# Kernel optimization log

Measured on AMD Instinct MI355X. Metric: run time of the kernel, lower is better.

## Reference

```python
import jax, jax.numpy as jnp
import numpy as np

B, S, D, H = 4, 4096, 512, 512


def setup_inputs() -> dict:
    key = jax.random.key(0)
    ks = jax.random.split(key, 11)
    def rn(k, shape):
        return jax.random.normal(k, shape, dtype=jnp.float32)
    return {
        "query": rn(ks[0], (B, 1, D)),
        "keys": rn(ks[1], (B, S, D)),
        "values": rn(ks[2], (B, S, D)),
        "Wq": rn(ks[3], (D, H)) / np.sqrt(D),
        "bq": rn(ks[4], (H,)) * 0.02,
        "Wk": rn(ks[5], (D, H)) / np.sqrt(D),
        "bk": rn(ks[6], (H,)) * 0.02,
        "Wv": rn(ks[7], (D, H)) / np.sqrt(D),
        "bv": rn(ks[8], (H,)) * 0.02,
        "Wo": rn(ks[9], (H, D)) / np.sqrt(H),
        "bo": rn(ks[10], (D,)) * 0.02,
    }


def reference(query, keys, values, Wq, bq, Wk, bk, Wv, bv, Wo, bo):
    # projections
    q = query @ Wq + bq      # (B, 1, H)
    k = keys @ Wk + bk       # (B, S, H)
    v = values @ Wv + bv     # (B, S, H)
    scale = jnp.sqrt(jnp.asarray(q.shape[-1], dtype=jnp.float32))
    # single-query scores: (B, 1, S)
    scores = jnp.einsum('bqh,bsh->bqs', q, k)
    seq = k.shape[1]
    # torch masked_fill broadcasts (B,1,S) against tril (1,S,S) -> (B,S,S)
    causal = jnp.tril(jnp.ones((seq, seq), dtype=bool))[None]  # (1, S, S)
    masked = jnp.where(causal, scores, -jnp.inf)                # (B, S, S)
    attn_weights = jax.nn.softmax(masked / scale, axis=-1)      # (B, S, S)
    context = jnp.einsum('brs,bsh->brh', attn_weights, v)       # (B, S, H)
    out = context @ Wo + bo                                     # (B, S, D)
    return out, attn_weights
```

## Files before the change

kernel.cpp:

```cpp
#include <hip/hip_runtime.h>
#include <hip/hip_bf16.h>

#define BB 4
#define SS 4096
#define DD 512
#define HH 512

typedef __attribute__((ext_vector_type(8))) short bf16x8;
typedef __attribute__((ext_vector_type(4))) float f32x4;

__global__ __launch_bounds__(256) void k_pre1(const float* __restrict__ query,
                                              const float* __restrict__ Wq,
                                              const float* __restrict__ bq,
                                              const float* __restrict__ Wv,
                                              const float* __restrict__ Wo,
                                              float* __restrict__ qv,
                                              float* __restrict__ Wvop) {
    __shared__ float smem[8320];
    int wb = blockIdx.x, tid = threadIdx.x;
    if (wb < 32) {
        float* qs = smem;
        float (*red)[64] = reinterpret_cast<float(*)[64]>(smem + 512);
        int hg = wb & 7, b = wb >> 3;
        int hl = tid & 63, qq = tid >> 6;
        int h = hg * 64 + hl;
        for (int d = tid; d < DD; d += 256) qs[d] = query[b * DD + d];
        __syncthreads();
        float a = 0.f;
        int d0 = qq * 128;
        for (int d = d0; d < d0 + 128; ++d)
            a += qs[d] * Wq[(size_t)d * HH + h];
        red[qq][hl] = a;
        __syncthreads();
        if (tid < 64)
            qv[b * HH + hg * 64 + tid] = red[0][tid] + red[1][tid] + red[2][tid] + red[3][tid]
                                       + bq[hg * 64 + tid];
    } else {
        int t = wb - 32;
        int hs = t >> 6, rem = t & 63;
        int n0 = (rem & 7) * 64, k0 = (rem >> 3) * 64;
        float (*lo)[65] = reinterpret_cast<float(*)[65]>(smem);
        float (*lv)[65] = reinterpret_cast<float(*)[65]>(smem + 4160);
        int tn = (tid & 15) * 4, tk = (tid >> 4) * 4;
        float acc[4][4] = {};
        int hbase = hs * 128;
        for (int h0 = hbase; h0 < hbase + 128; h0 += 64) {
            for (int i = tid; i < 64 * 64; i += 256) {
                int rr = i >> 6, cc = i & 63;
                lo[rr][cc] = Wo[(size_t)(h0 + rr) * DD + n0 + cc];
                lv[rr][cc] = Wv[(size_t)(k0 + rr) * HH + h0 + cc];
            }
            __syncthreads();
            for (int h = 0; h < 64; ++h)
#pragma unroll
                for (int a = 0; a < 4; ++a) {
                    float vv = lv[tk + a][h];
#pragma unroll
                    for (int c = 0; c < 4; ++c) acc[a][c] += vv * lo[h][tn + c];
                }
            __syncthreads();
        }
        float* dst = Wvop + (size_t)hs * (DD * HH);
        for (int a = 0; a < 4; ++a)
            for (int c = 0; c < 4; ++c)
                dst[(size_t)(k0 + tk + a) * DD + n0 + tn + c] = acc[a][c];
    }
}

__global__ __launch_bounds__(256) void k_pre2(const float* __restrict__ Wk,
                                              const float* __restrict__ qv,
                                              const float* __restrict__ bk,
                                              const float* __restrict__ Wvop,
                                              const float* __restrict__ bv,
                                              const float* __restrict__ Wo,
                                              const float* __restrict__ bo,
                                              float* __restrict__ wout,
                                              float* __restrict__ cq,
                                              __hip_bfloat16* __restrict__ WvoT,
                                              float* __restrict__ bfinal) {
    __shared__ float smem[4160];
    int wb = blockIdx.x, tid = threadIdx.x;
    if (wb < 512) {
        float* qs = smem;
        float* red = smem + 512;
        int b = wb >> 7, dg = wb & 127;
        int wid = tid >> 6, lane = tid & 63;
        for (int h = tid; h < HH; h += 256) qs[h] = qv[b * HH + h];
        __syncthreads();
        int d = dg * 4 + wid;
        const float4* row = reinterpret_cast<const float4*>(Wk + (size_t)d * HH);
        float4 r0 = row[lane * 2], r1 = row[lane * 2 + 1];
        int h = lane * 8;
        float acc = r0.x * qs[h] + r0.y * qs[h + 1] + r0.z * qs[h + 2] + r0.w * qs[h + 3]
                  + r1.x * qs[h + 4] + r1.y * qs[h + 5] + r1.z * qs[h + 6] + r1.w * qs[h + 7];
        for (int off = 32; off > 0; off >>= 1) acc += __shfl_down(acc, off);
        if (lane == 0) wout[b * DD + d] = acc;
        if (dg == 0) {
            red[tid] = qs[tid] * bk[tid] + qs[tid + 256] * bk[tid + 256];
            __syncthreads();
            for (int off = 128; off > 0; off >>= 1) {
                if (tid < off) red[tid] += red[tid + off];
                __syncthreads();
            }
            if (tid == 0) cq[b] = red[0];
        }
    } else if (wb < 576) {
        int t = wb - 512;
        int n0 = (t & 7) * 64, k0 = (t >> 3) * 64;
        float (*ts)[65] = reinterpret_cast<float(*)[65]>(smem);
#pragma unroll
        for (int i = 0; i < 16; ++i) {
            int idx = tid + i * 256;
            int kk = idx >> 6, nn = idx & 63;
            size_t off = (size_t)(k0 + kk) * DD + n0 + nn;
            float s = Wvop[off] + Wvop[(size_t)DD * HH + off]
                    + Wvop[2 * (size_t)DD * HH + off] + Wvop[3 * (size_t)DD * HH + off];
            ts[nn][kk] = s;
        }
        __syncthreads();
#pragma unroll
        for (int i = 0; i < 16; ++i) {
            int idx = tid + i * 256;
            int row = idx >> 6, col = idx & 63;
            WvoT[(size_t)(n0 + row) * DD + k0 + col] = __float2bfloat16(ts[row][col]);
        }
    } else {
        int n0 = (wb - 576) * 64;
        int nn = tid & 63, hs = tid >> 6;
        float acc = 0.f;
        for (int hh = 0; hh < 128; ++hh) {
            int h = hs * 128 + hh;
            acc += bv[h] * Wo[(size_t)h * DD + n0 + nn];
        }
        float (*red)[64] = reinterpret_cast<float(*)[64]>(smem);
        red[hs][nn] = acc;
        __syncthreads();
        if (tid < 64)
            bfinal[n0 + tid] = red[0][tid] + red[1][tid] + red[2][tid] + red[3][tid]
                             + bo[n0 + tid];
    }
}

__global__ __launch_bounds__(256) void k_scores_p(const float* __restrict__ keys,
                                                  const float* __restrict__ wv,
                                                  const float* __restrict__ cq,
                                                  float* __restrict__ p) {
    __shared__ float ws[DD];
    int wb = blockIdx.x, tid = threadIdx.x;
    int b = wb >> 10, sg = wb & 1023;
    int wid = tid >> 6, lane = tid & 63;
    for (int d = tid; d < DD; d += 256) ws[d] = wv[b * DD + d];
    __syncthreads();
    int s = sg * 4 + wid;
    const float4* row = reinterpret_cast<const float4*>(keys + ((size_t)b * SS + s) * DD);
    float4 r0 = row[lane * 2], r1 = row[lane * 2 + 1];
    int h = lane * 8;
    float acc = r0.x * ws[h] + r0.y * ws[h + 1] + r0.z * ws[h + 2] + r0.w * ws[h + 3]
              + r1.x * ws[h + 4] + r1.y * ws[h + 5] + r1.z * ws[h + 6] + r1.w * ws[h + 7];
    for (int off = 32; off > 0; off >>= 1) acc += __shfl_down(acc, off);
    const float inv_scale = 0.04419417382415922f;
    if (lane == 0) p[b * SS + s] = expf((acc + cq[b]) * inv_scale);
}

__global__ __launch_bounds__(64) void k_tile_scan(const float* __restrict__ values,
                                                  const float* __restrict__ p,
                                                  float* __restrict__ T64,
                                                  float* __restrict__ inv_cum) {
    int bx = blockIdx.x, tid = threadIdx.x;
    if (bx < 512) {
        __shared__ float ps[64];
        int b = bx >> 7, t = (bx >> 1) & 63, chunk = bx & 1;
        ps[tid] = p[b * SS + t * 64 + tid];
        __syncthreads();
        int d = chunk * 256 + tid * 4;
        const float* vp = values + ((size_t)b * SS + (size_t)t * 64) * DD + d;
        f32x4 acc = {0.f, 0.f, 0.f, 0.f};
        for (int i = 0; i < 64; ++i) {
            float4 v = *reinterpret_cast<const float4*>(vp + (size_t)i * DD);
            float pi = ps[i];
            acc[0] += pi * v.x; acc[1] += pi * v.y; acc[2] += pi * v.z; acc[3] += pi * v.w;
        }
        *reinterpret_cast<f32x4*>(&T64[((size_t)b * 64 + t) * DD + d]) = acc;
    } else {
        int b = bx - 512;
        const float* pb = p + (size_t)b * SS;
        float loc[64];
        float own = 0.f;
#pragma unroll
        for (int g = 0; g < 16; ++g) {
            float4 v = *reinterpret_cast<const float4*>(pb + tid * 64 + g * 4);
            loc[g * 4 + 0] = v.x; loc[g * 4 + 1] = v.y;
            loc[g * 4 + 2] = v.z; loc[g * 4 + 3] = v.w;
            own += v.x + v.y + v.z + v.w;
        }
        float incl = own;
        for (int off = 1; off < 64; off <<= 1) {
            float v = __shfl_up(incl, off);
            if (tid >= off) incl += v;
        }
        float run = incl - own;
        float* ib = inv_cum + (size_t)b * SS + tid * 64;
#pragma unroll
        for (int g = 0; g < 16; ++g) {
            float4 iv;
            run += loc[g * 4 + 0]; iv.x = 1.f / run;
            run += loc[g * 4 + 1]; iv.y = 1.f / run;
            run += loc[g * 4 + 2]; iv.z = 1.f / run;
            run += loc[g * 4 + 3]; iv.w = 1.f / run;
            *reinterpret_cast<float4*>(ib + g * 4) = iv;
        }
    }
}

__global__ __launch_bounds__(512) void k_fat(const float* __restrict__ values,
                                             const float* __restrict__ p,
                                             const float* __restrict__ icum,
                                             const float* __restrict__ T64,
                                             const __hip_bfloat16* __restrict__ Bt,
                                             const float* __restrict__ bfinal,
                                             float* __restrict__ Out,
                                             float* __restrict__ attn) {
    __shared__ __align__(16) short As[64][512];
    __shared__ float ps[64], ics[64];
    int bx = blockIdx.x, tid = threadIdx.x;
    if (bx < 256) {
        int b = bx >> 6, tb = bx & 63;
        int m0 = bx * 64;
        if (tid < 64) ps[tid] = p[b * SS + tb * 64 + tid];
        else if (tid < 128) ics[tid - 64] = icum[b * SS + tb * 64 + (tid - 64)];
        float acc = 0.f;
        for (int t = 0; t < tb; ++t) acc += T64[((size_t)b * 64 + t) * DD + tid];
        __syncthreads();
        const float* vp = values + ((size_t)b * SS + (size_t)tb * 64) * DD + tid;
        int gcol = tid >> 3, gsub = tid & 7;
        for (int i = 0; i < 64; ++i) {
            acc += ps[i] * vp[(size_t)i * DD];
            __hip_bfloat16 cv = __float2bfloat16(acc * ics[i]);
            short sv;
            __builtin_memcpy(&sv, &cv, 2);
            As[i][(((gcol ^ (i & 7)) << 3) | gsub)] = sv;
        }
        __syncthreads();
        int wv = tid >> 6, lane = tid & 63;
        int n0 = wv * 64;
        int lrow = lane & 15, lk = (lane >> 4) * 8;
        f32x4 oacc[4][4] = {};
        const short* Bp = reinterpret_cast<const short*>(Bt);
        for (int kk = 0; kk < 512; kk += 32) {
            int gbase = (kk + lk) >> 3;
            bf16x8 af[4], bfr[4];
#pragma unroll
            for (int i = 0; i < 4; ++i) {
                int row = i * 16 + lrow;
                af[i] = *reinterpret_cast<const bf16x8*>(&As[row][((gbase ^ (row & 7)) << 3)]);
            }
#pragma unroll
            for (int j = 0; j < 4; ++j)
                bfr[j] = *reinterpret_cast<const bf16x8*>(Bp + (size_t)(n0 + j * 16 + lrow) * 512 + kk + lk);
#pragma unroll
            for (int i = 0; i < 4; ++i)
#pragma unroll
                for (int j = 0; j < 4; ++j)
                    oacc[i][j] = __builtin_amdgcn_mfma_f32_16x16x32_bf16(af[i], bfr[j], oacc[i][j], 0, 0, 0);
        }
        int rbase = (lane >> 4) * 4;
        for (int i = 0; i < 4; ++i)
            for (int j = 0; j < 4; ++j) {
                int col = n0 + j * 16 + lrow;
                float bb = bfinal[col];
#pragma unroll
                for (int r = 0; r < 4; ++r) {
                    int row = m0 + i * 16 + rbase + r;
                    Out[(size_t)row * DD + col] = oacc[i][j][r] + bb;
                }
            }
    } else {
        int ab = bx - 256;
        int b = ab >> 9, rblk = ab & 511;
        int r0 = rblk * 8;
        const float* pb = p + b * SS;
        float4 pv[2];
        pv[0] = *reinterpret_cast<const float4*>(pb + tid * 4);
        pv[1] = *reinterpret_cast<const float4*>(pb + 2048 + tid * 4);
        const float* icb = icum + b * SS + r0;
#pragma unroll
        for (int row = 0; row < 8; ++row) {
            int r = r0 + row;
            float ic = icb[row];
            size_t base = ((size_t)b * SS + r) * SS;
#pragma unroll
            for (int g = 0; g < 2; ++g) {
                int s = g * 2048 + tid * 4;
                float4 o;
                o.x = (s + 0 <= r) ? pv[g].x * ic : 0.f;
                o.y = (s + 1 <= r) ? pv[g].y * ic : 0.f;
                o.z = (s + 2 <= r) ? pv[g].z * ic : 0.f;
                o.w = (s + 3 <= r) ? pv[g].w * ic : 0.f;
                *reinterpret_cast<float4*>(&attn[base + s]) = o;
            }
        }
    }
}

extern "C" void kernel_launch(void* const* d_in, const int* in_sizes, int n_in,
                              void* d_out, int out_size, void* d_ws, size_t ws_size,
                              hipStream_t stream) {
    const float* query  = (const float*)d_in[0];
    const float* keys   = (const float*)d_in[1];
    const float* values = (const float*)d_in[2];
    const float* Wq = (const float*)d_in[3];
    const float* bq = (const float*)d_in[4];
    const float* Wk = (const float*)d_in[5];
    const float* bk = (const float*)d_in[6];
    const float* Wv = (const float*)d_in[7];
    const float* bv = (const float*)d_in[8];
    const float* Wo = (const float*)d_in[9];
    const float* bo = (const float*)d_in[10];

    float* out  = (float*)d_out;
    float* attn = out + (size_t)BB * SS * DD;

    char* ws = (char*)d_ws;
    float* Wvop = (float*)(ws);
    __hip_bfloat16* WvoT = (__hip_bfloat16*)(ws + 4194304);
    float* T64  = (float*)(ws + 4718592);
    float* p    = (float*)(ws + 5242880);
    float* icum = (float*)(ws + 5308416);
    float* qv   = (float*)(ws + 5373952);
    float* wv   = (float*)(ws + 5382144);
    float* cq   = (float*)(ws + 5390336);
    float* bfin = (float*)(ws + 5390592);

    k_pre1     <<<288,   256, 0, stream>>>(query, Wq, bq, Wv, Wo, qv, Wvop);
    k_pre2     <<<584,   256, 0, stream>>>(Wk, qv, bk, Wvop, bv, Wo, bo, wv, cq, WvoT, bfin);
    k_scores_p <<<4096,  256, 0, stream>>>(keys, wv, cq, p);
    k_tile_scan<<<516,    64, 0, stream>>>(values, p, T64, icum);
    k_fat      <<<2304,  512, 0, stream>>>(values, p, icum, T64, WvoT, bfin, out, attn);
}
```

Measured before the change: 115.2 us.

## Merge pre-kernels and scores into fewer launches, widen tile-scan blocks

Computes q, cq and the Wk-projected query vector inside one block per batch in the first kernel, which removes the separate k_pre2 dot-product stage. The score/exp computation is fused into the same launch as the Wvo transpose and the bias reduction, with each block now handling 16 rows. The tile-scan kernel moves to 256-thread blocks covering full rows with float2 loads. This drops one kernel launch and its dependency boundary, but the q/Wk work now runs serially in only four blocks, which may lengthen the critical path.

```diff
diff --git a/kernel.cpp b/kernel.cpp
--- a/kernel.cpp
+++ b/kernel.cpp
@@ -9,34 +9,52 @@
 typedef __attribute__((ext_vector_type(8))) short bf16x8;
 typedef __attribute__((ext_vector_type(4))) float f32x4;
 
-__global__ __launch_bounds__(256) void k_pre1(const float* __restrict__ query,
-                                              const float* __restrict__ Wq,
-                                              const float* __restrict__ bq,
-                                              const float* __restrict__ Wv,
-                                              const float* __restrict__ Wo,
-                                              float* __restrict__ qv,
-                                              float* __restrict__ Wvop) {
+__global__ __launch_bounds__(256) void k_pre(const float* __restrict__ query,
+                                             const float* __restrict__ Wq,
+                                             const float* __restrict__ bq,
+                                             const float* __restrict__ Wk,
+                                             const float* __restrict__ bk,
+                                             const float* __restrict__ Wv,
+                                             const float* __restrict__ Wo,
+                                             float* __restrict__ wout,
+                                             float* __restrict__ cq,
+                                             float* __restrict__ Wvop) {
     __shared__ float smem[8320];
     int wb = blockIdx.x, tid = threadIdx.x;
-    if (wb < 32) {
-        float* qs = smem;
-        float (*red)[64] = reinterpret_cast<float(*)[64]>(smem + 512);
-        int hg = wb & 7, b = wb >> 3;
-        int hl = tid & 63, qq = tid >> 6;
-        int h = hg * 64 + hl;
-        for (int d = tid; d < DD; d += 256) qs[d] = query[b * DD + d];
-        __syncthreads();
-        float a = 0.f;
-        int d0 = qq * 128;
-        for (int d = d0; d < d0 + 128; ++d)
-            a += qs[d] * Wq[(size_t)d * HH + h];
-        red[qq][hl] = a;
-        __syncthreads();
-        if (tid < 64)
-            qv[b * HH + hg * 64 + tid] = red[0][tid] + red[1][tid] + red[2][tid] + red[3][tid]
-                                       + bq[hg * 64 + tid];
+    if (wb < 4) {
+        float* qs  = smem;
+        float* qo  = smem + 512;
+        float* red = smem + 1024;
+        int b = wb;
+        qs[tid] = query[b * DD + tid];
+        qs[tid + 256] = query[b * DD + tid + 256];
+        __syncthreads();
+        float a0 = bq[tid], a1 = bq[tid + 256];
+        for (int d = 0; d < DD; ++d) {
+            float qd = qs[d];
+            a0 += qd * Wq[(size_t)d * HH + tid];
+            a1 += qd * Wq[(size_t)d * HH + tid + 256];
+        }
+        qo[tid] = a0; qo[tid + 256] = a1;
+        red[tid] = a0 * bk[tid] + a1 * bk[tid + 256];
+        __syncthreads();
+        for (int off = 128; off > 0; off >>= 1) {
+            if (tid < off) red[tid] += red[tid + off];
+            __syncthreads();
+        }
+        if (tid == 0) cq[b] = red[0];
+        float w0 = 0.f, w1 = 0.f;
+        const float* wk0 = Wk + (size_t)tid * HH;
+        const float* wk1 = Wk + (size_t)(tid + 256) * HH;
+        for (int h = 0; h < HH; ++h) {
+            float qh = qo[h];
+            w0 += qh * wk0[h];
+            w1 += qh * wk1[h];
+        }
+        wout[b * DD + tid] = w0;
+        wout[b * DD + tid + 256] = w1;
     } else {
-        int t = wb - 32;
+        int t = wb - 4;
         int hs = t >> 6, rem = t & 63;
         int n0 = (rem & 7) * 64, k0 = (rem >> 3) * 64;
         float (*lo)[65] = reinterpret_cast<float(*)[65]>(smem);
@@ -67,45 +85,39 @@
     }
 }
 
-__global__ __launch_bounds__(256) void k_pre2(const float* __restrict__ Wk,
-                                              const float* __restrict__ qv,
-                                              const float* __restrict__ bk,
-                                              const float* __restrict__ Wvop,
-                                              const float* __restrict__ bv,
-                                              const float* __restrict__ Wo,
-                                              const float* __restrict__ bo,
-                                              float* __restrict__ wout,
-                                              float* __restrict__ cq,
-                                              __hip_bfloat16* __restrict__ WvoT,
-                                              float* __restrict__ bfinal) {
+__global__ __launch_bounds__(256) void k_scores_wr(const float* __restrict__ keys,
+                                                   const float* __restrict__ wv,
+                                                   const float* __restrict__ cq,
+                                                   const float* __restrict__ Wvop,
+                                                   const float* __restrict__ bv,
+                                                   const float* __restrict__ Wo,
+                                                   const float* __restrict__ bo,
+                                                   float* __restrict__ p,
+                                                   __hip_bfloat16* __restrict__ WvoT,
+                                                   float* __restrict__ bfinal) {
     __shared__ float smem[4160];
     int wb = blockIdx.x, tid = threadIdx.x;
-    if (wb < 512) {
-        float* qs = smem;
-        float* red = smem + 512;
-        int b = wb >> 7, dg = wb & 127;
+    if (wb < 1024) {
+        float* ws = smem;
+        int b = wb >> 8, sg = wb & 255;
         int wid = tid >> 6, lane = tid & 63;
-        for (int h = tid; h < HH; h += 256) qs[h] = qv[b * HH + h];
-        __syncthreads();
-        int d = dg * 4 + wid;
-        const float4* row = reinterpret_cast<const float4*>(Wk + (size_t)d * HH);
-        float4 r0 = row[lane * 2], r1 = row[lane * 2 + 1];
+        for (int d = tid; d < DD; d += 256) ws[d] = wv[b * DD + d];
+        __syncthreads();
+        const float inv_scale = 0.04419417382415922f;
+        float cqb = cq[b];
         int h = lane * 8;
-        float acc = r0.x * qs[h] + r0.y * qs[h + 1] + r0.z * qs[h + 2] + r0.w * qs[h + 3]
-                  + r1.x * qs[h + 4] + r1.y * qs[h + 5] + r1.z * qs[h + 6] + r1.w * qs[h + 7];
-        for (int off = 32; off > 0; off >>= 1) acc += __shfl_down(acc, off);
-        if (lane == 0) wout[b * DD + d] = acc;
-        if (dg == 0) {
-            red[tid] = qs[tid] * bk[tid] + qs[tid + 256] * bk[tid + 256];
-            __syncthreads();
-            for (int off = 128; off > 0; off >>= 1) {
-                if (tid < off) red[tid] += red[tid + off];
-                __syncthreads();
-            }
-            if (tid == 0) cq[b] = red[0];
-        }
-    } else if (wb < 576) {
-        int t = wb - 512;
+#pragma unroll
+        for (int rr = 0; rr < 4; ++rr) {
+            int s = sg * 16 + wid * 4 + rr;
+            const float4* row = reinterpret_cast<const float4*>(keys + ((size_t)b * SS + s) * DD);
+            float4 r0 = row[lane * 2], r1 = row[lane * 2 + 1];
+            float acc = r0.x * ws[h] + r0.y * ws[h + 1] + r0.z * ws[h + 2] + r0.w * ws[h + 3]
+                      + r1.x * ws[h + 4] + r1.y * ws[h + 5] + r1.z * ws[h + 6] + r1.w * ws[h + 7];
+            for (int off = 32; off > 0; off >>= 1) acc += __shfl_down(acc, off);
+            if (lane == 0) p[b * SS + s] = expf((acc + cqb) * inv_scale);
+        }
+    } else if (wb < 1088) {
+        int t = wb - 1024;
         int n0 = (t & 7) * 64, k0 = (t >> 3) * 64;
         float (*ts)[65] = reinterpret_cast<float(*)[65]>(smem);
 #pragma unroll
@@ -125,7 +137,7 @@
             WvoT[(size_t)(n0 + row) * DD + k0 + col] = __float2bfloat16(ts[row][col]);
         }
     } else {
-        int n0 = (wb - 576) * 64;
+        int n0 = (wb - 1088) * 64;
         int nn = tid & 63, hs = tid >> 6;
         float acc = 0.f;
         for (int hh = 0; hh < 128; ++hh) {
@@ -141,48 +153,27 @@
     }
 }
 
-__global__ __launch_bounds__(256) void k_scores_p(const float* __restrict__ keys,
-                                                  const float* __restrict__ wv,
-                                                  const float* __restrict__ cq,
-                                                  float* __restrict__ p) {
-    __shared__ float ws[DD];
-    int wb = blockIdx.x, tid = threadIdx.x;
-    int b = wb >> 10, sg = wb & 1023;
-    int wid = tid >> 6, lane = tid & 63;
-    for (int d = tid; d < DD; d += 256) ws[d] = wv[b * DD + d];
-    __syncthreads();
-    int s = sg * 4 + wid;
-    const float4* row = reinterpret_cast<const float4*>(keys + ((size_t)b * SS + s) * DD);
-    float4 r0 = row[lane * 2], r1 = row[lane * 2 + 1];
-    int h = lane * 8;
-    float acc = r0.x * ws[h] + r0.y * ws[h + 1] + r0.z * ws[h + 2] + r0.w * ws[h + 3]
-              + r1.x * ws[h + 4] + r1.y * ws[h + 5] + r1.z * ws[h + 6] + r1.w * ws[h + 7];
-    for (int off = 32; off > 0; off >>= 1) acc += __shfl_down(acc, off);
-    const float inv_scale = 0.04419417382415922f;
-    if (lane == 0) p[b * SS + s] = expf((acc + cq[b]) * inv_scale);
-}
-
-__global__ __launch_bounds__(64) void k_tile_scan(const float* __restrict__ values,
-                                                  const float* __restrict__ p,
-                                                  float* __restrict__ T64,
-                                                  float* __restrict__ inv_cum) {
+__global__ __launch_bounds__(256) void k_tile_scan(const float* __restrict__ values,
+                                                   const float* __restrict__ p,
+                                                   float* __restrict__ T64,
+                                                   float* __restrict__ inv_cum) {
     int bx = blockIdx.x, tid = threadIdx.x;
-    if (bx < 512) {
+    if (bx < 256) {
         __shared__ float ps[64];
-        int b = bx >> 7, t = (bx >> 1) & 63, chunk = bx & 1;
-        ps[tid] = p[b * SS + t * 64 + tid];
-        __syncthreads();
-        int d = chunk * 256 + tid * 4;
-        const float* vp = values + ((size_t)b * SS + (size_t)t * 64) * DD + d;
-        f32x4 acc = {0.f, 0.f, 0.f, 0.f};
+        int b = bx >> 6, t = bx & 63;
+        if (tid < 64) ps[tid] = p[b * SS + t * 64 + tid];
+        __syncthreads();
+        const float* vp = values + ((size_t)b * SS + (size_t)t * 64) * DD + tid * 2;
+        float ax = 0.f, ay = 0.f;
         for (int i = 0; i < 64; ++i) {
-            float4 v = *reinterpret_cast<const float4*>(vp + (size_t)i * DD);
+            float2 v = *reinterpret_cast<const float2*>(vp + (size_t)i * DD);
             float pi = ps[i];
-            acc[0] += pi * v.x; acc[1] += pi * v.y; acc[2] += pi * v.z; acc[3] += pi * v.w;
-        }
-        *reinterpret_cast<f32x4*>(&T64[((size_t)b * 64 + t) * DD + d]) = acc;
-    } else {
-        int b = bx - 512;
+            ax += pi * v.x; ay += pi * v.y;
+        }
+        float2 o; o.x = ax; o.y = ay;
+        *reinterpret_cast<float2*>(&T64[((size_t)b * 64 + t) * DD + tid * 2]) = o;
+    } else if (tid < 64) {
+        int b = bx - 256;
         const float* pb = p + (size_t)b * SS;
         float loc[64];
         float own = 0.f;
@@ -326,14 +317,12 @@
     float* T64  = (float*)(ws + 4718592);
     float* p    = (float*)(ws + 5242880);
     float* icum = (float*)(ws + 5308416);
-    float* qv   = (float*)(ws + 5373952);
-    float* wv   = (float*)(ws + 5382144);
-    float* cq   = (float*)(ws + 5390336);
-    float* bfin = (float*)(ws + 5390592);
-
-    k_pre1     <<<288,   256, 0, stream>>>(query, Wq, bq, Wv, Wo, qv, Wvop);
-    k_pre2     <<<584,   256, 0, stream>>>(Wk, qv, bk, Wvop, bv, Wo, bo, wv, cq, WvoT, bfin);
-    k_scores_p <<<4096,  256, 0, stream>>>(keys, wv, cq, p);
-    k_tile_scan<<<516,    64, 0, stream>>>(values, p, T64, icum);
-    k_fat      <<<2304,  512, 0, stream>>>(values, p, icum, T64, WvoT, bfin, out, attn);
-}
+    float* wv   = (float*)(ws + 5373952);
+    float* cq   = (float*)(ws + 5382144);
+    float* bfin = (float*)(ws + 5382400);
+
+    k_pre       <<<260,   256, 0, stream>>>(query, Wq, bq, Wk, bk, Wv, Wo, wv, cq, Wvop);
+    k_scores_wr <<<1096,  256, 0, stream>>>(keys, wv, cq, Wvop, bv, Wo, bo, p, WvoT, bfin);
+    k_tile_scan <<<260,   256, 0, stream>>>(values, p, T64, icum);
+    k_fat       <<<2304,  512, 0, stream>>>(values, p, icum, T64, WvoT, bfin, out, attn);
+}
```

Measured after the change: 166.6 us. +44.7%, slower.
